# Optimization experiments

Hardware: AMD Instinct MI355X
Metric: run time of the kernel (lower is better)

## Reference

```python
import jax, jax.numpy as jnp
import numpy as np

N_NODES = 50000
N_EDGES = 800000
D = 128


def gcn_conv(x, edge_index, W, b, num_nodes):
    # PyG GCNConv: h = D^{-1/2} (A + I) D^{-1/2} (x @ W) + b
    xw = x @ W  # [N, D]
    src, dst = edge_index[0], edge_index[1]
    loop = jnp.arange(num_nodes, dtype=src.dtype)
    src = jnp.concatenate([src, loop])
    dst = jnp.concatenate([dst, loop])
    deg = jax.ops.segment_sum(jnp.ones_like(dst, dtype=xw.dtype), dst,
                              num_segments=num_nodes)  # [N]
    dinv = jnp.where(deg > 0, jax.lax.rsqrt(deg), 0.0)
    norm = dinv[src] * dinv[dst]  # [E+N]
    msg = xw[src] * norm[:, None]  # gather + scale, [E+N, D]
    agg = jax.ops.segment_sum(msg, dst, num_segments=num_nodes)  # scatter-add
    return agg + b


def setup_inputs() -> dict:
    key = jax.random.key(0)
    ks = jax.random.split(key, 8)
    s = 1.0 / np.sqrt(D)
    return {
        "x": jax.random.normal(ks[0], (N_NODES, D), dtype=jnp.float32),
        "edge_index": jax.random.randint(ks[1], (2, N_EDGES), 0, N_NODES, dtype=jnp.int32),
        "Wg": jax.random.normal(ks[2], (D, D), dtype=jnp.float32) * s,
        "bg": jnp.zeros((D,), dtype=jnp.float32),
        "W1": jax.random.normal(ks[3], (D, 128), dtype=jnp.float32) * s,
        "b1": jnp.zeros((128,), dtype=jnp.float32),
        "W2": jax.random.normal(ks[4], (128, 64), dtype=jnp.float32) * (1.0 / np.sqrt(128)),
        "b2": jnp.zeros((64,), dtype=jnp.float32),
        "W3": jax.random.normal(ks[5], (64, 2), dtype=jnp.float32) * (1.0 / np.sqrt(64)),
        "b3": jnp.zeros((2,), dtype=jnp.float32),
    }


def reference(x, edge_index, Wg, bg, W1, b1, W2, b2, W3, b3):
    out = jax.nn.relu(gcn_conv(x, edge_index, Wg, bg, x.shape[0]))
    h = out + x  # residual
    h = jax.nn.relu(h @ W1 + b1)
    h = jax.nn.relu(h @ W2 + b2)
    h = h @ W3 + b3  # [N, 2]
    return (h[:, 0], h[:, 1])
```

## Files before the change

### kernel.cpp

```cpp
#include <hip/hip_runtime.h>

#define TD 256
#define BCAP 3072
#define BINB 384
#define SWZB 8
#define XWB  640

typedef unsigned int uint;
typedef unsigned short ushort;
typedef __attribute__((ext_vector_type(8))) short bf16x8;
typedef __attribute__((ext_vector_type(4))) float f32x4;

__device__ __forceinline__ ushort f2bf(float f) {
    uint u = __float_as_uint(f);
    u += 0x7fffu + ((u >> 16) & 1u);
    return (ushort)(u >> 16);
}
__device__ __forceinline__ float2 bfp2f(uint u) {
    float2 r;
    r.x = __uint_as_float(u << 16);
    r.y = __uint_as_float(u & 0xffff0000u);
    return r;
}

__global__ __launch_bounds__(256) void k_front(
        const float* __restrict__ Wg, const float* __restrict__ W1,
        const float* __restrict__ W2,
        ushort* __restrict__ W1f, ushort* __restrict__ W2f,
        const float* __restrict__ x, ushort* __restrict__ xws,
        const int* __restrict__ src, const int* __restrict__ dst, int e,
        int nbuck, int* __restrict__ bucketCursor, uint* __restrict__ binned,
        int n, int nt16) {
    __shared__ __align__(16) ushort sW[16384];
    int t = threadIdx.x;

    if (blockIdx.x < BINB) {
        int* hist = (int*)sW;
        int* base = hist + 512;
        int* cur  = base + 512;
        int per = (e + BINB - 1) / BINB;
        int e0 = blockIdx.x * per;
        int e1 = min(e0 + per, e);
        for (int i = t; i < nbuck; i += TD) hist[i] = 0;
        __syncthreads();
        for (int i = e0 + t; i < e1; i += TD)
            atomicAdd(&hist[dst[i] >> 7], 1);
        __syncthreads();
        for (int i = t; i < nbuck; i += TD) {
            int c = hist[i];
            base[i] = (c > 0) ? atomicAdd(&bucketCursor[i], c) : 0;
            cur[i] = 0;
        }
        __syncthreads();
        for (int i = e0 + t; i < e1; i += TD) {
            int d = dst[i];
            int b = d >> 7;
            int pos = base[b] + atomicAdd(&cur[b], 1);
            if (pos < BCAP)
                binned[(size_t)b * BCAP + pos] = ((uint)src[i] << 7) | (uint)(d & 127);
        }
        return;
    }

    if (blockIdx.x < BINB + SWZB) {
        int tid0 = (blockIdx.x - BINB) * TD + t;
        int stride = SWZB * TD;
        for (int id = tid0; id < 2048; id += stride) {
            int lane = id & 63;
            int col = ((id >> 8) << 4) + (lane & 15);
            int k0 = ((id >> 6) & 3) * 32 + (lane >> 4) * 8;
            #pragma unroll
            for (int j = 0; j < 8; j++)
                W1f[id * 8 + j] = f2bf(W1[(k0 + j) * 128 + col]);
        }
        for (int id = tid0; id < 1024; id += stride) {
            int lane = id & 63;
            int col = ((id >> 8) << 4) + (lane & 15);
            int k0 = ((id >> 6) & 3) * 32 + (lane >> 4) * 8;
            #pragma unroll
            for (int j = 0; j < 8; j++)
                W2f[id * 8 + j] = f2bf(W2[(k0 + j) * 64 + col]);
        }
        return;
    }

    for (int id = t; id < 2048; id += TD) {
        int lane = id & 63;
        int col = ((id >> 8) << 4) + (lane & 15);
        int k0 = ((id >> 6) & 3) * 32 + (lane >> 4) * 8;
        union { bf16x8 v; ushort u[8]; } tmp;
        #pragma unroll
        for (int j = 0; j < 8; j++)
            tmp.u[j] = f2bf(Wg[(k0 + j) * 128 + col]);
        *(bf16x8*)&sW[id * 8] = tmp.v;
    }
    __syncthreads();

    int xwid = blockIdx.x - (BINB + SWZB);
    int nxw = gridDim.x - (BINB + SWZB);
    int wave = t >> 6, lane = t & 63;
    int quad = lane >> 4, m = lane & 15;

    for (int tile = xwid * 4 + wave; tile < nt16; tile += nxw * 4) {
        int row0 = tile * 16;
        int arow = min(row0 + m, n - 1);
        const float* pa = x + (size_t)arow * 128 + quad * 8;
        bf16x8 af[4];
        #pragma unroll
        for (int kc = 0; kc < 4; kc++) {
            float4 f0 = *(const float4*)(pa + kc * 32);
            float4 f1 = *(const float4*)(pa + kc * 32 + 4);
            union { bf16x8 v; ushort u[8]; } tmp;
            tmp.u[0] = f2bf(f0.x); tmp.u[1] = f2bf(f0.y);
            tmp.u[2] = f2bf(f0.z); tmp.u[3] = f2bf(f0.w);
            tmp.u[4] = f2bf(f1.x); tmp.u[5] = f2bf(f1.y);
            tmp.u[6] = f2bf(f1.z); tmp.u[7] = f2bf(f1.w);
            af[kc] = tmp.v;
        }
        #pragma unroll
        for (int c16 = 0; c16 < 8; c16++) {
            f32x4 acc = {0.f, 0.f, 0.f, 0.f};
            #pragma unroll
            for (int kc = 0; kc < 4; kc++) {
                bf16x8 bf = *(const bf16x8*)&sW[((c16 * 4 + kc) * 64 + lane) * 8];
                acc = __builtin_amdgcn_mfma_f32_16x16x32_bf16(af[kc], bf, acc, 0, 0, 0);
            }
            int col = c16 * 16 + m;
            #pragma unroll
            for (int i = 0; i < 4; i++) {
                int r = row0 + quad * 4 + i;
                if (r < n)
                    xws[(size_t)r * 128 + col] = f2bf(acc[i]);
            }
        }
    }
}

__global__ __launch_bounds__(256) void kb_fill(const int* __restrict__ counts,
                                               const uint* __restrict__ binned,
                                               int n, int nbuck,
                                               int* __restrict__ deg,
                                               int* __restrict__ rowStart,
                                               float* __restrict__ dinv,
                                               int* __restrict__ csr) {
    __shared__ int d128[128];
    __shared__ int sc[128];
    __shared__ int rs128[128];
    __shared__ int cur128[128];
    __shared__ int wsum[4];
    int b = blockIdx.x;
    int t = threadIdx.x;

    int part = 0;
    for (int i = t; i < b; i += TD) part += counts[i];
    #pragma unroll
    for (int m = 1; m < 64; m <<= 1) part += __shfl_xor(part, m);
    if ((t & 63) == 0) wsum[t >> 6] = part;
    if (t < 128) { d128[t] = 0; cur128[t] = 0; }
    __syncthreads();
    int base = wsum[0] + wsum[1] + wsum[2] + wsum[3];
    int cnt = min(counts[b], BCAP);
    int node0 = b << 7;

    for (int i = t; i < cnt; i += TD)
        atomicAdd(&d128[binned[(size_t)b * BCAP + i] & 127], 1);
    __syncthreads();
    int v = (t < 128) ? d128[t] : 0;
    if (t < 128) sc[t] = v;
    __syncthreads();
    for (int off = 1; off < 128; off <<= 1) {
        int u = (t < 128 && t >= off) ? sc[t - off] : 0;
        __syncthreads();
        if (t < 128) sc[t] += u;
        __syncthreads();
    }
    if (t < 128) {
        int node = node0 + t;
        if (node < n) {
            int rs = base + sc[t] - v;
            rs128[t] = rs;
            rowStart[node] = rs;
            deg[node] = v;
            dinv[node] = rsqrtf((float)(v + 1));
        }
    }
    __syncthreads();
    for (int i = t; i < cnt; i += TD) {
        uint pk = binned[(size_t)b * BCAP + i];
        int loc = pk & 127;
        int slot = rs128[loc] + atomicAdd(&cur128[loc], 1);
        csr[slot] = (int)(pk >> 7);
    }
}

__global__ __launch_bounds__(256) void k_agg(const uint* __restrict__ xws,
                                             const float* __restrict__ x,
                                             const int* __restrict__ rowStart,
                                             const int* __restrict__ deg,
                                             const int* __restrict__ csr,
                                             const float* __restrict__ dinv,
                                             const float* __restrict__ bg,
                                             ushort* __restrict__ h0b, int n) {
    int wave = threadIdx.x >> 6;
    int lane = threadIdx.x & 63;
    int node = blockIdx.x * 4 + wave;
    if (node >= n) return;
    float dv = dinv[node];
    float2 A0, A1 = {0.f,0.f}, A2 = {0.f,0.f}, A3 = {0.f,0.f};
    {
        float2 s = bfp2f(xws[(size_t)node * 64 + lane]);
        A0.x = dv * s.x; A0.y = dv * s.y;
    }
    int st = rowStart[node];
    int cnt = deg[node];
    int i = 0;
    for (; i + 8 <= cnt; i += 8) {
        int s0 = csr[st + i + 0], s1 = csr[st + i + 1];
        int s2 = csr[st + i + 2], s3 = csr[st + i + 3];
        int s4 = csr[st + i + 4], s5 = csr[st + i + 5];
        int s6 = csr[st + i + 6], s7 = csr[st + i + 7];
        float d0 = dinv[s0], d1 = dinv[s1], d2 = dinv[s2], d3 = dinv[s3];
        float d4 = dinv[s4], d5 = dinv[s5], d6 = dinv[s6], d7 = dinv[s7];
        uint u0 = xws[(size_t)s0 * 64 + lane];
        uint u1 = xws[(size_t)s1 * 64 + lane];
        uint u2 = xws[(size_t)s2 * 64 + lane];
        uint u3 = xws[(size_t)s3 * 64 + lane];
        uint u4 = xws[(size_t)s4 * 64 + lane];
        uint u5 = xws[(size_t)s5 * 64 + lane];
        uint u6 = xws[(size_t)s6 * 64 + lane];
        uint u7 = xws[(size_t)s7 * 64 + lane];
        float2 v0 = bfp2f(u0), v1 = bfp2f(u1), v2 = bfp2f(u2), v3 = bfp2f(u3);
        float2 v4 = bfp2f(u4), v5 = bfp2f(u5), v6 = bfp2f(u6), v7 = bfp2f(u7);
        A0.x = fmaf(d0, v0.x, A0.x); A0.y = fmaf(d0, v0.y, A0.y);
        A1.x = fmaf(d1, v1.x, A1.x); A1.y = fmaf(d1, v1.y, A1.y);
        A2.x = fmaf(d2, v2.x, A2.x); A2.y = fmaf(d2, v2.y, A2.y);
        A3.x = fmaf(d3, v3.x, A3.x); A3.y = fmaf(d3, v3.y, A3.y);
        A0.x = fmaf(d4, v4.x, A0.x); A0.y = fmaf(d4, v4.y, A0.y);
        A1.x = fmaf(d5, v5.x, A1.x); A1.y = fmaf(d5, v5.y, A1.y);
        A2.x = fmaf(d6, v6.x, A2.x); A2.y = fmaf(d6, v6.y, A2.y);
        A3.x = fmaf(d7, v7.x, A3.x); A3.y = fmaf(d7, v7.y, A3.y);
    }
    for (; i < cnt; i++) {
        int s = csr[st + i];
        float ds = dinv[s];
        float2 v = bfp2f(xws[(size_t)s * 64 + lane]);
        A0.x = fmaf(ds, v.x, A0.x); A0.y = fmaf(ds, v.y, A0.y);
    }
    float2 acc;
    acc.x = (A0.x + A1.x) + (A2.x + A3.x);
    acc.y = (A0.y + A1.y) + (A2.y + A3.y);
    float2 b = ((const float2*)bg)[lane];
    float2 xv = ((const float2*)x)[(size_t)node * 64 + lane];
    float ox = fmaxf(acc.x * dv + b.x, 0.f) + xv.x;
    float oy = fmaxf(acc.y * dv + b.y, 0.f) + xv.y;
    uint up = ((uint)f2bf(oy) << 16) | (uint)f2bf(ox);
    ((uint*)h0b)[(size_t)node * 64 + lane] = up;
}

__global__ __launch_bounds__(256) void k_mlp(const ushort* __restrict__ h0b,
                                             const ushort* __restrict__ W1f,
                                             const ushort* __restrict__ W2f,
                                             const float* __restrict__ b1,
                                             const float* __restrict__ b2,
                                             const float* __restrict__ W3,
                                             const float* __restrict__ b3,
                                             float* __restrict__ out,
                                             int n, int nt16) {
    __shared__ __align__(16) ushort sW1[16384];
    __shared__ __align__(16) ushort tb[4][16 * 136];
    int t = threadIdx.x;
    for (int i = t; i < 2048; i += TD)
        ((float4*)sW1)[i] = ((const float4*)W1f)[i];
    __syncthreads();

    int wave = t >> 6, lane = t & 63;
    int quad = lane >> 4, m = lane & 15;
    ushort* tw = &tb[wave][0];

    float bc1[8];
    #pragma unroll
    for (int c = 0; c < 8; c++) bc1[c] = b1[c * 16 + m];
    float bc2[4], w30[4], w31[4];
    #pragma unroll
    for (int c = 0; c < 4; c++) {
        int col = c * 16 + m;
        bc2[c] = b2[col];
        w30[c] = W3[col * 2 + 0];
        w31[c] = W3[col * 2 + 1];
    }
    float b30 = b3[0], b31 = b3[1];

    for (int tile = blockIdx.x * 4 + wave; tile < nt16; tile += gridDim.x * 4) {
        int row0 = tile * 16;
        int arow = min(row0 + m, n - 1);
        const ushort* pa = h0b + (size_t)arow * 128 + quad * 8;
        bf16x8 af[4];
        #pragma unroll
        for (int kc = 0; kc < 4; kc++)
            af[kc] = *(const bf16x8*)(pa + kc * 32);

        #pragma unroll
        for (int c16 = 0; c16 < 8; c16++) {
            f32x4 acc = {0.f, 0.f, 0.f, 0.f};
            #pragma unroll
            for (int kc = 0; kc < 4; kc++) {
                bf16x8 bf = *(const bf16x8*)&sW1[((c16 * 4 + kc) * 64 + lane) * 8];
                acc = __builtin_amdgcn_mfma_f32_16x16x32_bf16(af[kc], bf, acc, 0, 0, 0);
            }
            int col = c16 * 16 + m;
            #pragma unroll
            for (int i = 0; i < 4; i++)
                tw[(quad * 4 + i) * 136 + col] = f2bf(fmaxf(acc[i] + bc1[c16], 0.f));
        }

        bf16x8 a2[4];
        #pragma unroll
        for (int kc = 0; kc < 4; kc++)
            a2[kc] = *(const bf16x8*)&tw[m * 136 + kc * 32 + quad * 8];

        float p0[4] = {}, p1[4] = {};
        #pragma unroll
        for (int c16 = 0; c16 < 4; c16++) {
            f32x4 acc = {0.f, 0.f, 0.f, 0.f};
            #pragma unroll
            for (int kc = 0; kc < 4; kc++) {
                bf16x8 bf = *(const bf16x8*)&W2f[((c16 * 4 + kc) * 64 + lane) * 8];
                acc = __builtin_amdgcn_mfma_f32_16x16x32_bf16(a2[kc], bf, acc, 0, 0, 0);
            }
            #pragma unroll
            for (int i = 0; i < 4; i++) {
                float h2 = fmaxf(acc[i] + bc2[c16], 0.f);
                p0[i] += h2 * w30[c16];
                p1[i] += h2 * w31[c16];
            }
        }
        #pragma unroll
        for (int i = 0; i < 4; i++) {
            #pragma unroll
            for (int msk = 1; msk < 16; msk <<= 1) {
                p0[i] += __shfl_xor(p0[i], msk);
                p1[i] += __shfl_xor(p1[i], msk);
            }
        }
        if (m == 0) {
            #pragma unroll
            for (int i = 0; i < 4; i++) {
                int r = row0 + quad * 4 + i;
                if (r < n) {
                    out[r] = p0[i] + b30;
                    out[(size_t)n + r] = p1[i] + b31;
                }
            }
        }
    }
}


extern "C" void kernel_launch(void* const* d_in, const int* in_sizes, int n_in,
                              void* d_out, int out_size, void* d_ws, size_t ws_size,
                              hipStream_t stream) {
    const float* x  = (const float*)d_in[0];
    const int*   ei = (const int*)d_in[1];
    const float* Wg = (const float*)d_in[2];
    const float* bg = (const float*)d_in[3];
    const float* W1 = (const float*)d_in[4];
    const float* b1 = (const float*)d_in[5];
    const float* W2 = (const float*)d_in[6];
    const float* b2 = (const float*)d_in[7];
    const float* W3 = (const float*)d_in[8];
    const float* b3 = (const float*)d_in[9];
    float* out = (float*)d_out;

    int n = in_sizes[0] / 128;
    int e = in_sizes[1] / 2;
    const int* src = ei;
    const int* dst = ei + e;

    char* ws = (char*)d_ws;
    size_t off = 0;
    auto alloc = [&](size_t bytes) -> void* {
        void* p = ws + off;
        off = (off + bytes + 255) & ~(size_t)255;
        return p;
    };
    int nbuck = (n + 127) >> 7;
    int*    deg      = (int*)alloc(sizeof(int) * (size_t)n);
    int*    rowStart = (int*)alloc(sizeof(int) * (size_t)n);
    float*  dinv     = (float*)alloc(sizeof(float) * (size_t)n);
    int*    bucketCursor = (int*)alloc(sizeof(int) * 512);
    uint*   binned   = (uint*)alloc(sizeof(uint) * (size_t)nbuck * BCAP);
    int*    csr      = (int*)alloc(sizeof(int) * (size_t)e);
    ushort* xws      = (ushort*)alloc(sizeof(ushort) * (size_t)n * 128);
    ushort* h0b      = (ushort*)alloc(sizeof(ushort) * (size_t)n * 128);
    ushort* W1f      = (ushort*)alloc(sizeof(ushort) * 16384);
    ushort* W2f      = (ushort*)alloc(sizeof(ushort) * 8192);
    (void)ws_size; (void)n_in; (void)out_size;

    int nt16 = (n + 15) / 16;

    hipMemsetAsync(bucketCursor, 0, sizeof(int) * 512, stream);
    hipLaunchKernelGGL(k_front, dim3(BINB + SWZB + XWB), dim3(TD), 0, stream,
                       Wg, W1, W2, W1f, W2f, x, xws,
                       src, dst, e, nbuck, bucketCursor, binned, n, nt16);
    hipLaunchKernelGGL(kb_fill, dim3(nbuck), dim3(TD), 0, stream,
                       bucketCursor, binned, n, nbuck, deg, rowStart, dinv, csr);
    hipLaunchKernelGGL(k_agg,   dim3((n + 3) / 4), dim3(TD), 0, stream,
                       (const uint*)xws, x, rowStart, deg, csr, dinv, bg, h0b, n);
    hipLaunchKernelGGL(k_mlp,   dim3(784), dim3(TD), 0, stream,
                       h0b, W1f, W2f, b1, b2, W3, b3, out, n, nt16);
}
```

Measured before the change: 174.0 us.

## Split aggregation into four column passes with 16-lane groups per node

The aggregation kernel now processes the 128-column feature rows in four 32-column passes, one pass per group of blocks, with 16 lanes per node and 16 nodes per block. Each pass gathers a quarter of every source row, so the randomly accessed working set of each pass shrinks to a quarter of the xw table. The aim is better L2 or last-level cache hit rates. In exchange, every CSR index and dinv value is loaded four times, each gather moves only 64 bytes per row, and the unroll depth drops to 4.

New measurement: 188.4 us. +8.2%, slower.

```diff
diff --git a/kernel.cpp b/kernel.cpp
--- a/kernel.cpp
+++ b/kernel.cpp
@@ -200,61 +200,54 @@
                                              const int* __restrict__ csr,
                                              const float* __restrict__ dinv,
                                              const float* __restrict__ bg,
-                                             ushort* __restrict__ h0b, int n) {
-    int wave = threadIdx.x >> 6;
-    int lane = threadIdx.x & 63;
-    int node = blockIdx.x * 4 + wave;
+                                             ushort* __restrict__ h0b,
+                                             int n, int bpp) {
+    int pass = blockIdx.x / bpp;
+    int bi   = blockIdx.x % bpp;
+    int t = threadIdx.x;
+    int slot = t >> 4;
+    int lane = t & 15;
+    int node = bi * 16 + slot;
     if (node >= n) return;
+    int cb = pass * 16;
+
     float dv = dinv[node];
-    float2 A0, A1 = {0.f,0.f}, A2 = {0.f,0.f}, A3 = {0.f,0.f};
+    float2 A0, A1 = {0.f, 0.f};
     {
-        float2 s = bfp2f(xws[(size_t)node * 64 + lane]);
+        float2 s = bfp2f(xws[(size_t)node * 64 + cb + lane]);
         A0.x = dv * s.x; A0.y = dv * s.y;
     }
     int st = rowStart[node];
     int cnt = deg[node];
     int i = 0;
-    for (; i + 8 <= cnt; i += 8) {
+    for (; i + 4 <= cnt; i += 4) {
         int s0 = csr[st + i + 0], s1 = csr[st + i + 1];
         int s2 = csr[st + i + 2], s3 = csr[st + i + 3];
-        int s4 = csr[st + i + 4], s5 = csr[st + i + 5];
-        int s6 = csr[st + i + 6], s7 = csr[st + i + 7];
         float d0 = dinv[s0], d1 = dinv[s1], d2 = dinv[s2], d3 = dinv[s3];
-        float d4 = dinv[s4], d5 = dinv[s5], d6 = dinv[s6], d7 = dinv[s7];
-        uint u0 = xws[(size_t)s0 * 64 + lane];
-        uint u1 = xws[(size_t)s1 * 64 + lane];
-        uint u2 = xws[(size_t)s2 * 64 + lane];
-        uint u3 = xws[(size_t)s3 * 64 + lane];
-        uint u4 = xws[(size_t)s4 * 64 + lane];
-        uint u5 = xws[(size_t)s5 * 64 + lane];
-        uint u6 = xws[(size_t)s6 * 64 + lane];
-        uint u7 = xws[(size_t)s7 * 64 + lane];
+        uint u0 = xws[(size_t)s0 * 64 + cb + lane];
+        uint u1 = xws[(size_t)s1 * 64 + cb + lane];
+        uint u2 = xws[(size_t)s2 * 64 + cb + lane];
+        uint u3 = xws[(size_t)s3 * 64 + cb + lane];
         float2 v0 = bfp2f(u0), v1 = bfp2f(u1), v2 = bfp2f(u2), v3 = bfp2f(u3);
-        float2 v4 = bfp2f(u4), v5 = bfp2f(u5), v6 = bfp2f(u6), v7 = bfp2f(u7);
         A0.x = fmaf(d0, v0.x, A0.x); A0.y = fmaf(d0, v0.y, A0.y);
         A1.x = fmaf(d1, v1.x, A1.x); A1.y = fmaf(d1, v1.y, A1.y);
-        A2.x = fmaf(d2, v2.x, A2.x); A2.y = fmaf(d2, v2.y, A2.y);
-        A3.x = fmaf(d3, v3.x, A3.x); A3.y = fmaf(d3, v3.y, A3.y);
-        A0.x = fmaf(d4, v4.x, A0.x); A0.y = fmaf(d4, v4.y, A0.y);
-        A1.x = fmaf(d5, v5.x, A1.x); A1.y = fmaf(d5, v5.y, A1.y);
-        A2.x = fmaf(d6, v6.x, A2.x); A2.y = fmaf(d6, v6.y, A2.y);
-        A3.x = fmaf(d7, v7.x, A3.x); A3.y = fmaf(d7, v7.y, A3.y);
+        A0.x = fmaf(d2, v2.x, A0.x); A0.y = fmaf(d2, v2.y, A0.y);
+        A1.x = fmaf(d3, v3.x, A1.x); A1.y = fmaf(d3, v3.y, A1.y);
     }
     for (; i < cnt; i++) {
         int s = csr[st + i];
         float ds = dinv[s];
-        float2 v = bfp2f(xws[(size_t)s * 64 + lane]);
+        float2 v = bfp2f(xws[(size_t)s * 64 + cb + lane]);
         A0.x = fmaf(ds, v.x, A0.x); A0.y = fmaf(ds, v.y, A0.y);
     }
-    float2 acc;
-    acc.x = (A0.x + A1.x) + (A2.x + A3.x);
-    acc.y = (A0.y + A1.y) + (A2.y + A3.y);
-    float2 b = ((const float2*)bg)[lane];
-    float2 xv = ((const float2*)x)[(size_t)node * 64 + lane];
-    float ox = fmaxf(acc.x * dv + b.x, 0.f) + xv.x;
-    float oy = fmaxf(acc.y * dv + b.y, 0.f) + xv.y;
+    float ax = A0.x + A1.x;
+    float ay = A0.y + A1.y;
+    float2 b = ((const float2*)bg)[cb + lane];
+    float2 xv = ((const float2*)x)[(size_t)node * 64 + cb + lane];
+    float ox = fmaxf(ax * dv + b.x, 0.f) + xv.x;
+    float oy = fmaxf(ay * dv + b.y, 0.f) + xv.y;
     uint up = ((uint)f2bf(oy) << 16) | (uint)f2bf(ox);
-    ((uint*)h0b)[(size_t)node * 64 + lane] = up;
+    ((uint*)h0b)[(size_t)node * 64 + cb + lane] = up;
 }
 
 __global__ __launch_bounds__(256) void k_mlp(const ushort* __restrict__ h0b,
@@ -397,6 +390,7 @@
     (void)ws_size; (void)n_in; (void)out_size;
 
     int nt16 = (n + 15) / 16;
+    int bpp  = (n + 15) / 16;
 
     hipMemsetAsync(bucketCursor, 0, sizeof(int) * 512, stream);
     hipLaunchKernelGGL(k_front, dim3(BINB + SWZB + XWB), dim3(TD), 0, stream,
@@ -404,8 +398,8 @@
                        src, dst, e, nbuck, bucketCursor, binned, n, nt16);
     hipLaunchKernelGGL(kb_fill, dim3(nbuck), dim3(TD), 0, stream,
                        bucketCursor, binned, n, nbuck, deg, rowStart, dinv, csr);
-    hipLaunchKernelGGL(k_agg,   dim3((n + 3) / 4), dim3(TD), 0, stream,
-                       (const uint*)xws, x, rowStart, deg, csr, dinv, bg, h0b, n);
+    hipLaunchKernelGGL(k_agg,   dim3(bpp * 4), dim3(TD), 0, stream,
+                       (const uint*)xws, x, rowStart, deg, csr, dinv, bg, h0b, n, bpp);
     hipLaunchKernelGGL(k_mlp,   dim3(784), dim3(TD), 0, stream,
                        h0b, W1f, W2f, b1, b2, W3, b3, out, n, nt16);
 }
```
